# Performance work log

Measured on AMD Instinct MI355X. Metric: run time of the kernel, lower is better.

Reference implementation:

```python
import jax, jax.numpy as jnp
import numpy as np

D_MODEL = 1024
N_HEADS = 16
D_K = D_MODEL // N_HEADS


def setup_inputs() -> dict:
    key = jax.random.key(0)
    ks = jax.random.split(key, 11)
    B, S = 2, 2048
    scale = 1.0 / np.sqrt(D_MODEL)
    inp = {
        "Q_in": jax.random.normal(ks[0], (B, S, D_MODEL), jnp.float32),
        "K_in": jax.random.normal(ks[1], (B, S, D_MODEL), jnp.float32),
        "V_in": jax.random.normal(ks[2], (B, S, D_MODEL), jnp.float32),
        # torch nn.Linear convention: y = x @ W.T + b, W shape [out, in]
        "W_q": jax.random.normal(ks[3], (D_MODEL, D_MODEL), jnp.float32) * scale,
        "b_q": jax.random.normal(ks[4], (D_MODEL,), jnp.float32) * scale,
        "W_k": jax.random.normal(ks[5], (D_MODEL, D_MODEL), jnp.float32) * scale,
        "b_k": jax.random.normal(ks[6], (D_MODEL,), jnp.float32) * scale,
        "W_v": jax.random.normal(ks[7], (D_MODEL, D_MODEL), jnp.float32) * scale,
        "b_v": jax.random.normal(ks[8], (D_MODEL,), jnp.float32) * scale,
        "W_o": jax.random.normal(ks[9], (D_MODEL, D_MODEL), jnp.float32) * scale,
        "b_o": jax.random.normal(ks[10], (D_MODEL,), jnp.float32) * scale,
    }
    return inp


def reference(Q_in, K_in, V_in, W_q, b_q, W_k, b_k, W_v, b_v, W_o, b_o):
    B, S, _ = Q_in.shape

    def proj(x, W, b):
        # [B,S,D] -> [B,H,S,dk]
        y = x @ W.T + b
        return y.reshape(B, S, N_HEADS, D_K).transpose(0, 2, 1, 3)

    Q = proj(Q_in, W_q, b_q)
    K = proj(K_in, W_k, b_k)
    V = proj(V_in, W_v, b_v)

    scores = jnp.einsum("bhqd,bhkd->bhqk", Q, K) / jnp.sqrt(jnp.float32(D_K))
    attn_weights = jax.nn.softmax(scores, axis=-1)
    ctx = jnp.einsum("bhqk,bhkd->bhqd", attn_weights, V)
    ctx = ctx.transpose(0, 2, 1, 3).reshape(B, S, D_MODEL)
    output = ctx @ W_o.T + b_o
    return output, attn_weights
```

## Files before the change

kernel.cpp:

```cpp
#include <hip/hip_runtime.h>
#include <hip/hip_bf16.h>
#include <stdint.h>

typedef __attribute__((ext_vector_type(8))) short short8;
typedef __attribute__((ext_vector_type(4))) short short4v;
typedef __attribute__((ext_vector_type(4))) float f32x4;
typedef __attribute__((ext_vector_type(2))) float f32x2;

#define MFMA16x16x32(A, B, C) __builtin_amdgcn_mfma_f32_16x16x32_bf16((A), (B), (C), 0, 0, 0)

static constexpr int kS  = 2048;
static constexpr int kD  = 1024;
static constexpr int kDK = 64;

static constexpr size_t OFF_XQ  = 0;
static constexpr size_t OFF_XK  = 4194304;
static constexpr size_t OFF_XV  = 8388608;
static constexpr size_t OFF_W   = 12582912;
static constexpr size_t OFF_QP  = 16777216;
static constexpr size_t OFF_KP  = 20971520;
static constexpr size_t OFF_VT  = 25165824;
static constexpr size_t OFF_CTX = 29360128;

__device__ __forceinline__ short f2bf(float f) {
  __hip_bfloat16 h = __float2bfloat16(f);
  return *reinterpret_cast<short*>(&h);
}

__global__ __launch_bounds__(256) void cvt_kernel(
    const float* __restrict__ xq, const float* __restrict__ xk, const float* __restrict__ xv,
    const float* __restrict__ wq, const float* __restrict__ wk, const float* __restrict__ wv,
    const float* __restrict__ wo, __hip_bfloat16* __restrict__ dst)
{
  int g = blockIdx.x * 256 + threadIdx.x;
  const float* src;
  __hip_bfloat16* d;
  int rel;
  if (g < 3145728) {
    int seg = g >> 20; rel = g & 1048575;
    src = seg == 0 ? xq : (seg == 1 ? xk : xv);
    d = dst + (size_t)seg * 4194304;
  } else {
    int g2 = g - 3145728; int seg = g2 >> 18; rel = g2 & 262143;
    src = seg == 0 ? wq : (seg == 1 ? wk : (seg == 2 ? wv : wo));
    d = dst + OFF_W + (size_t)seg * 1048576;
  }
  float4 v = ((const float4*)src)[rel];
  short4v o;
  o.x = f2bf(v.x); o.y = f2bf(v.y); o.z = f2bf(v.z); o.w = f2bf(v.w);
  ((short4v*)d)[rel] = o;
}

__device__ __forceinline__ void stage_tile(short* lds, const __hip_bfloat16* g0, int t) {
  #pragma unroll
  for (int c = 0; c < 2; ++c) {
    const int e = t * 8 + c * 2048;
    const int row = e >> 5;
    const int kk = e & 31;
    __builtin_amdgcn_global_load_lds(
        (const __attribute__((address_space(1))) void*)(g0 + (size_t)row * kD + kk),
        (__attribute__((address_space(3))) void*)(lds + e), 16, 0, 0);
  }
}

__device__ __forceinline__ void gemm_main(const __hip_bfloat16* X, const __hip_bfloat16* W,
                                          short* As, short* Bs, f32x4 acc[4][4])
{
  const int t = threadIdx.x;
  const int lane = t & 63;
  const int wv = t >> 6;
  const int wr = wv >> 1, wc = wv & 1;
  const int fr = lane & 15;
  const int fc = (lane >> 4) * 8;
  for (int k0 = 0; k0 < kD; k0 += 32) {
    stage_tile(As, X + k0, t);
    stage_tile(Bs, W + k0, t);
    __syncthreads();
    short8 af[4], bfv[4];
    #pragma unroll
    for (int i = 0; i < 4; ++i) af[i]  = *(const short8*)&As[(wr * 64 + i * 16 + fr) * 32 + fc];
    #pragma unroll
    for (int i = 0; i < 4; ++i) bfv[i] = *(const short8*)&Bs[(wc * 64 + i * 16 + fr) * 32 + fc];
    #pragma unroll
    for (int i = 0; i < 4; ++i)
      #pragma unroll
      for (int j = 0; j < 4; ++j)
        acc[i][j] = MFMA16x16x32(af[i], bfv[j], acc[i][j]);
    __syncthreads();
  }
}

__global__ __launch_bounds__(256) void qkv_gemm(
    const __hip_bfloat16* __restrict__ Xq, const __hip_bfloat16* __restrict__ Xk,
    const __hip_bfloat16* __restrict__ Xv, const __hip_bfloat16* __restrict__ Wbase,
    const float* __restrict__ bq, const float* __restrict__ bk, const float* __restrict__ bv,
    __hip_bfloat16* __restrict__ Qp, __hip_bfloat16* __restrict__ Kp,
    __hip_bfloat16* __restrict__ Vt)
{
  __shared__ __align__(16) short As[128 * 32];
  __shared__ __align__(16) short Bs[128 * 32];
  const int z  = blockIdx.z;
  const int m0 = blockIdx.y * 128, n0 = blockIdx.x * 128;
  const __hip_bfloat16* X = (z == 0 ? Xq : (z == 1 ? Xk : Xv)) + (size_t)m0 * kD;
  const __hip_bfloat16* W = Wbase + (size_t)z * (kD * kD) + (size_t)n0 * kD;
  const float* bias = (z == 0 ? bq : (z == 1 ? bk : bv));
  f32x4 acc[4][4] = {};
  gemm_main(X, W, As, Bs, acc);

  const int lane = threadIdx.x & 63;
  const int wv = threadIdx.x >> 6;
  const int wr = wv >> 1, wc = wv & 1;
  short* dstQK = (short*)(z == 0 ? Qp : Kp);
  short* dstV  = (short*)Vt;
  #pragma unroll
  for (int i = 0; i < 4; ++i) {
    #pragma unroll
    for (int j = 0; j < 4; ++j) {
      #pragma unroll
      for (int r = 0; r < 4; ++r) {
        int m = m0 + wr * 64 + i * 16 + (lane >> 4) * 4 + r;
        int n = n0 + wc * 64 + j * 16 + (lane & 15);
        float y = acc[i][j][r] + bias[n];
        if (z == 0) y *= 0.125f;
        int b = m >> 11, sq = m & 2047, h = n >> 6, d = n & 63;
        if (z < 2)
          dstQK[((size_t)(b * 16 + h) * kS + sq) * kDK + d] = f2bf(y);
        else
          dstV[((size_t)(b * 16 + h) * kDK + d) * kS + sq] = f2bf(y);
      }
    }
  }
}

__global__ __launch_bounds__(256) void o_gemm(
    const __hip_bfloat16* __restrict__ Ctx, const __hip_bfloat16* __restrict__ Wo,
    const float* __restrict__ bo, float* __restrict__ out)
{
  __shared__ __align__(16) short As[128 * 32];
  __shared__ __align__(16) short Bs[128 * 32];
  const int m0 = blockIdx.y * 128, n0 = blockIdx.x * 128;
  f32x4 acc[4][4] = {};
  gemm_main(Ctx + (size_t)m0 * kD, Wo + (size_t)n0 * kD, As, Bs, acc);

  const int lane = threadIdx.x & 63;
  const int wv = threadIdx.x >> 6;
  const int wr = wv >> 1, wc = wv & 1;
  #pragma unroll
  for (int i = 0; i < 4; ++i) {
    #pragma unroll
    for (int j = 0; j < 4; ++j) {
      #pragma unroll
      for (int r = 0; r < 4; ++r) {
        int m = m0 + wr * 64 + i * 16 + (lane >> 4) * 4 + r;
        int n = n0 + wc * 64 + j * 16 + (lane & 15);
        __builtin_nontemporal_store(acc[i][j][r] + bo[n], &out[(size_t)m * kD + n]);
      }
    }
  }
}

__global__ __launch_bounds__(256) void attn_pass1(
    const __hip_bfloat16* __restrict__ Qp, const __hip_bfloat16* __restrict__ Kp,
    const __hip_bfloat16* __restrict__ Vt, __hip_bfloat16* __restrict__ Ctx,
    float* __restrict__ rinvp)
{
  __shared__ __align__(16) short Ks[2][32][68];
  __shared__ __align__(16) short Vs[2][64][36];
  __shared__ __align__(16) short Ps[4][16][36];
  const int t = threadIdx.x;
  const int lane = t & 63;
  const int w = t >> 6;
  const int fr = lane & 15;
  const int g4 = lane >> 4;
  const int fc = g4 * 8;

  const int id  = blockIdx.x;
  const int swz = (id & 7) * 128 + (id >> 3);
  const int bh  = swz >> 5;
  const int q0  = (swz & 31) * 64 + w * 16;

  const __hip_bfloat16* Qh = Qp + (size_t)bh * kS * kDK;
  const __hip_bfloat16* Kh = Kp + (size_t)bh * kS * kDK;
  const __hip_bfloat16* Vh = Vt + (size_t)bh * kDK * kS;

  const short8 qf0 = *(const short8*)(Qh + (size_t)(q0 + fr) * kDK + fc);
  const short8 qf1 = *(const short8*)(Qh + (size_t)(q0 + fr) * kDK + 32 + fc);

  const int kr = t >> 3, kc = (t & 7) * 8;
  const int vr = t >> 2, vc = (t & 3) * 8;

  f32x4 ctxacc[4] = {};
  float ssumq = 0.f;

  short8 kA, vA, kB, vB;

#define LOAD_T(KREG, VREG, TI)                                                   \
  KREG = *(const short8*)(Kh + (size_t)((TI) * 32 + kr) * kDK + kc);             \
  VREG = *(const short8*)(Vh + (size_t)vr * kS + (TI) * 32 + vc);

#define STORE_T(KREG, VREG, BUF)                                                 \
  *(short8*)&Ks[BUF][kr][kc] = KREG;                                             \
  *(short8*)&Vs[BUF][vr][vc] = VREG;

#define COMPUTE_T(BUF)                                                           \
  {                                                                              \
    short8 k0a = *(const short8*)&Ks[BUF][fr][fc];                               \
    short8 k0b = *(const short8*)&Ks[BUF][fr][32 + fc];                          \
    short8 k1a = *(const short8*)&Ks[BUF][16 + fr][fc];                          \
    short8 k1b = *(const short8*)&Ks[BUF][16 + fr][32 + fc];                     \
    f32x4 s0 = {}; s0 = MFMA16x16x32(k0a, qf0, s0); s0 = MFMA16x16x32(k0b, qf1, s0); \
    f32x4 s1 = {}; s1 = MFMA16x16x32(k1a, qf0, s1); s1 = MFMA16x16x32(k1b, qf1, s1); \
    float e00 = __expf(s0[0]), e01 = __expf(s0[1]);                              \
    float e02 = __expf(s0[2]), e03 = __expf(s0[3]);                              \
    float e10 = __expf(s1[0]), e11 = __expf(s1[1]);                              \
    float e12 = __expf(s1[2]), e13 = __expf(s1[3]);                              \
    ssumq += (e00 + e01) + (e02 + e03) + (e10 + e11) + (e12 + e13);              \
    short4v p0, p1;                                                              \
    p0.x = f2bf(e00); p0.y = f2bf(e01); p0.z = f2bf(e02); p0.w = f2bf(e03);      \
    p1.x = f2bf(e10); p1.y = f2bf(e11); p1.z = f2bf(e12); p1.w = f2bf(e13);      \
    *(short4v*)&Ps[w][fr][g4 * 4]      = p0;                                     \
    *(short4v*)&Ps[w][fr][16 + g4 * 4] = p1;                                     \
    short8 pf = *(const short8*)&Ps[w][fr][fc];                                  \
    _Pragma("unroll")                                                            \
    for (int dc = 0; dc < 4; ++dc) {                                             \
      short8 vf = *(const short8*)&Vs[BUF][dc * 16 + fr][fc];                    \
      ctxacc[dc] = MFMA16x16x32(pf, vf, ctxacc[dc]);                             \
    }                                                                            \
  }

  LOAD_T(kA, vA, 0);
  STORE_T(kA, vA, 0);
  LOAD_T(kB, vB, 1);
  __syncthreads();

  for (int i = 0; i < 64; i += 2) {
    COMPUTE_T(0);
    STORE_T(kB, vB, 1);
    if (i + 2 < 64) { LOAD_T(kA, vA, i + 2); }
    __syncthreads();
    COMPUTE_T(1);
    if (i + 2 < 64) { STORE_T(kA, vA, 0); }
    if (i + 3 < 64) { LOAD_T(kB, vB, i + 3); }
    __syncthreads();
  }

  float s = ssumq;
  s += __shfl_xor(s, 16);
  s += __shfl_xor(s, 32);
  const float rvq = 1.0f / s;
  if (g4 == 0) rinvp[(size_t)bh * kS + q0 + fr] = rvq;

  float rinv4[4];
  #pragma unroll
  for (int j = 0; j < 4; ++j) rinv4[j] = __shfl(rvq, g4 * 4 + j, 16);

  const int b = bh >> 4, h = bh & 15;
  #pragma unroll
  for (int dc = 0; dc < 4; ++dc) {
    #pragma unroll
    for (int j = 0; j < 4; ++j) {
      int r = g4 * 4 + j;
      float v = ctxacc[dc][j] * rinv4[j];
      ((short*)Ctx)[((size_t)(b * kS + q0 + r)) * kD + h * kDK + dc * 16 + fr] = f2bf(v);
    }
  }
#undef LOAD_T
#undef STORE_T
#undef COMPUTE_T
}

__global__ __launch_bounds__(256) void attn_pass2(
    const __hip_bfloat16* __restrict__ Qp, const __hip_bfloat16* __restrict__ Kp,
    const float* __restrict__ rinvp, float* __restrict__ Aw)
{
  const int t = threadIdx.x;
  const int lane = t & 63;
  const int w = t >> 6;
  const int fr = lane & 15;
  const int g4 = lane >> 4;
  const int fc = g4 * 8;

  const int id  = blockIdx.x;
  const int swz = (id & 7) * 512 + (id >> 3);
  const int bh  = swz >> 7;
  const int ksg = (swz >> 5) & 3;
  const int q0  = (swz & 31) * 64 + w * 16;
  const int k0  = ksg * 512;

  const __hip_bfloat16* Qh = Qp + (size_t)bh * kS * kDK;
  const __hip_bfloat16* Kh = Kp + (size_t)bh * kS * kDK;

  const short8 qf0 = *(const short8*)(Qh + (size_t)(q0 + fr) * kDK + fc);
  const short8 qf1 = *(const short8*)(Qh + (size_t)(q0 + fr) * kDK + 32 + fc);

  const float rvq = rinvp[(size_t)bh * kS + q0 + fr];
  float* aw = Aw + ((size_t)bh * kS + q0 + fr) * kS;

  short8 ka[8], kb[8];

#define LOADK(ARR, KT_)                                                          \
  _Pragma("unroll")                                                              \
  for (int c = 0; c < 4; ++c) {                                                  \
    ARR[2 * c]     = *(const short8*)(Kh + (size_t)((KT_) + c * 16 + fr) * kDK + fc);      \
    ARR[2 * c + 1] = *(const short8*)(Kh + (size_t)((KT_) + c * 16 + fr) * kDK + 32 + fc); \
  }

#define CSTORE(ARR, KT_)                                                         \
  _Pragma("unroll")                                                              \
  for (int c = 0; c < 4; ++c) {                                                  \
    f32x4 st = {};                                                               \
    st = MFMA16x16x32(ARR[2 * c], qf0, st);                                      \
    st = MFMA16x16x32(ARR[2 * c + 1], qf1, st);                                  \
    f32x4 v;                                                                     \
    _Pragma("unroll")                                                            \
    for (int j = 0; j < 4; ++j) v[j] = __expf(st[j]) * rvq;                      \
    __builtin_nontemporal_store(v, (f32x4*)(aw + (KT_) + c * 16 + g4 * 4));      \
  }

  LOADK(ka, k0);
  for (int kt = k0; kt < k0 + 512; kt += 128) {
    LOADK(kb, kt + 64);
    CSTORE(ka, kt);
    if (kt + 128 < k0 + 512) { LOADK(ka, kt + 128); }
    CSTORE(kb, kt + 64);
  }
#undef LOADK
#undef CSTORE
}

extern "C" void kernel_launch(void* const* d_in, const int* in_sizes, int n_in,
                              void* d_out, int out_size, void* d_ws, size_t ws_size,
                              hipStream_t stream) {
  (void)in_sizes; (void)n_in; (void)out_size; (void)ws_size;
  const float* Qin = (const float*)d_in[0];
  const float* Kin = (const float*)d_in[1];
  const float* Vin = (const float*)d_in[2];
  const float* Wq  = (const float*)d_in[3];
  const float* bq  = (const float*)d_in[4];
  const float* Wk  = (const float*)d_in[5];
  const float* bk  = (const float*)d_in[6];
  const float* Wv  = (const float*)d_in[7];
  const float* bv  = (const float*)d_in[8];
  const float* Wo  = (const float*)d_in[9];
  const float* bo  = (const float*)d_in[10];
  __hip_bfloat16* ws = (__hip_bfloat16*)d_ws;
  float* out = (float*)d_out;
  float* rinvp = (float*)(ws + OFF_XQ);

  cvt_kernel<<<16384, 256, 0, stream>>>(Qin, Kin, Vin, Wq, Wk, Wv, Wo, ws);
  qkv_gemm<<<dim3(8, 32, 3), 256, 0, stream>>>(
      ws + OFF_XQ, ws + OFF_XK, ws + OFF_XV, ws + OFF_W, bq, bk, bv,
      ws + OFF_QP, ws + OFF_KP, ws + OFF_VT);
  attn_pass1<<<1024, 256, 0, stream>>>(
      ws + OFF_QP, ws + OFF_KP, ws + OFF_VT, ws + OFF_CTX, rinvp);
  attn_pass2<<<4096, 256, 0, stream>>>(
      ws + OFF_QP, ws + OFF_KP, rinvp, out + 4194304);
  o_gemm<<<dim3(8, 32), 256, 0, stream>>>(
      ws + OFF_CTX, ws + OFF_W + 3 * 1048576, bo, out);
}
```

Measured before the change: 298.8 us.

## Load K/V directly into registers in attention pass and fuse O-GEMM with pass2

```diff
diff --git a/kernel.cpp b/kernel.cpp
--- a/kernel.cpp
+++ b/kernel.cpp
@@ -132,40 +132,11 @@
   }
 }
 
-__global__ __launch_bounds__(256) void o_gemm(
-    const __hip_bfloat16* __restrict__ Ctx, const __hip_bfloat16* __restrict__ Wo,
-    const float* __restrict__ bo, float* __restrict__ out)
-{
-  __shared__ __align__(16) short As[128 * 32];
-  __shared__ __align__(16) short Bs[128 * 32];
-  const int m0 = blockIdx.y * 128, n0 = blockIdx.x * 128;
-  f32x4 acc[4][4] = {};
-  gemm_main(Ctx + (size_t)m0 * kD, Wo + (size_t)n0 * kD, As, Bs, acc);
-
-  const int lane = threadIdx.x & 63;
-  const int wv = threadIdx.x >> 6;
-  const int wr = wv >> 1, wc = wv & 1;
-  #pragma unroll
-  for (int i = 0; i < 4; ++i) {
-    #pragma unroll
-    for (int j = 0; j < 4; ++j) {
-      #pragma unroll
-      for (int r = 0; r < 4; ++r) {
-        int m = m0 + wr * 64 + i * 16 + (lane >> 4) * 4 + r;
-        int n = n0 + wc * 64 + j * 16 + (lane & 15);
-        __builtin_nontemporal_store(acc[i][j][r] + bo[n], &out[(size_t)m * kD + n]);
-      }
-    }
-  }
-}
-
 __global__ __launch_bounds__(256) void attn_pass1(
     const __hip_bfloat16* __restrict__ Qp, const __hip_bfloat16* __restrict__ Kp,
     const __hip_bfloat16* __restrict__ Vt, __hip_bfloat16* __restrict__ Ctx,
     float* __restrict__ rinvp)
 {
-  __shared__ __align__(16) short Ks[2][32][68];
-  __shared__ __align__(16) short Vs[2][64][36];
   __shared__ __align__(16) short Ps[4][16][36];
   const int t = threadIdx.x;
   const int lane = t & 63;
@@ -186,30 +157,24 @@
   const short8 qf0 = *(const short8*)(Qh + (size_t)(q0 + fr) * kDK + fc);
   const short8 qf1 = *(const short8*)(Qh + (size_t)(q0 + fr) * kDK + 32 + fc);
 
-  const int kr = t >> 3, kc = (t & 7) * 8;
-  const int vr = t >> 2, vc = (t & 3) * 8;
-
   f32x4 ctxacc[4] = {};
   float ssumq = 0.f;
 
-  short8 kA, vA, kB, vB;
-
-#define LOAD_T(KREG, VREG, TI)                                                   \
-  KREG = *(const short8*)(Kh + (size_t)((TI) * 32 + kr) * kDK + kc);             \
-  VREG = *(const short8*)(Vh + (size_t)vr * kS + (TI) * 32 + vc);
-
-#define STORE_T(KREG, VREG, BUF)                                                 \
-  *(short8*)&Ks[BUF][kr][kc] = KREG;                                             \
-  *(short8*)&Vs[BUF][vr][vc] = VREG;
-
-#define COMPUTE_T(BUF)                                                           \
+  short8 kA[4], vA[4], kB[4], vB[4];
+
+#define LOAD32(KR, VR, KT_)                                                      \
+  KR[0] = *(const short8*)(Kh + (size_t)((KT_) + fr) * kDK + fc);                \
+  KR[1] = *(const short8*)(Kh + (size_t)((KT_) + fr) * kDK + 32 + fc);           \
+  KR[2] = *(const short8*)(Kh + (size_t)((KT_) + 16 + fr) * kDK + fc);           \
+  KR[3] = *(const short8*)(Kh + (size_t)((KT_) + 16 + fr) * kDK + 32 + fc);      \
+  _Pragma("unroll")                                                              \
+  for (int dc = 0; dc < 4; ++dc)                                                 \
+    VR[dc] = *(const short8*)(Vh + (size_t)(dc * 16 + fr) * kS + (KT_) + fc);
+
+#define COMPUTE32(KR, VR)                                                        \
   {                                                                              \
-    short8 k0a = *(const short8*)&Ks[BUF][fr][fc];                               \
-    short8 k0b = *(const short8*)&Ks[BUF][fr][32 + fc];                          \
-    short8 k1a = *(const short8*)&Ks[BUF][16 + fr][fc];                          \
-    short8 k1b = *(const short8*)&Ks[BUF][16 + fr][32 + fc];                     \
-    f32x4 s0 = {}; s0 = MFMA16x16x32(k0a, qf0, s0); s0 = MFMA16x16x32(k0b, qf1, s0); \
-    f32x4 s1 = {}; s1 = MFMA16x16x32(k1a, qf0, s1); s1 = MFMA16x16x32(k1b, qf1, s1); \
+    f32x4 s0 = {}; s0 = MFMA16x16x32(KR[0], qf0, s0); s0 = MFMA16x16x32(KR[1], qf1, s0); \
+    f32x4 s1 = {}; s1 = MFMA16x16x32(KR[2], qf0, s1); s1 = MFMA16x16x32(KR[3], qf1, s1); \
     float e00 = __expf(s0[0]), e01 = __expf(s0[1]);                              \
     float e02 = __expf(s0[2]), e03 = __expf(s0[3]);                              \
     float e10 = __expf(s1[0]), e11 = __expf(s1[1]);                              \
@@ -222,27 +187,19 @@
     *(short4v*)&Ps[w][fr][16 + g4 * 4] = p1;                                     \
     short8 pf = *(const short8*)&Ps[w][fr][fc];                                  \
     _Pragma("unroll")                                                            \
-    for (int dc = 0; dc < 4; ++dc) {                                             \
-      short8 vf = *(const short8*)&Vs[BUF][dc * 16 + fr][fc];                    \
-      ctxacc[dc] = MFMA16x16x32(pf, vf, ctxacc[dc]);                             \
-    }                                                                            \
-  }
-
-  LOAD_T(kA, vA, 0);
-  STORE_T(kA, vA, 0);
-  LOAD_T(kB, vB, 1);
-  __syncthreads();
-
-  for (int i = 0; i < 64; i += 2) {
-    COMPUTE_T(0);
-    STORE_T(kB, vB, 1);
-    if (i + 2 < 64) { LOAD_T(kA, vA, i + 2); }
-    __syncthreads();
-    COMPUTE_T(1);
-    if (i + 2 < 64) { STORE_T(kA, vA, 0); }
-    if (i + 3 < 64) { LOAD_T(kB, vB, i + 3); }
-    __syncthreads();
-  }
+    for (int dc = 0; dc < 4; ++dc)                                               \
+      ctxacc[dc] = MFMA16x16x32(pf, VR[dc], ctxacc[dc]);                         \
+  }
+
+  LOAD32(kA, vA, 0);
+  for (int kt = 0; kt < kS; kt += 64) {
+    LOAD32(kB, vB, kt + 32);
+    COMPUTE32(kA, vA);
+    if (kt + 64 < kS) { LOAD32(kA, vA, kt + 64); }
+    COMPUTE32(kB, vB);
+  }
+#undef LOAD32
+#undef COMPUTE32
 
   float s = ssumq;
   s += __shfl_xor(s, 16);
@@ -264,15 +221,16 @@
       ((short*)Ctx)[((size_t)(b * kS + q0 + r)) * kD + h * kDK + dc * 16 + fr] = f2bf(v);
     }
   }
-#undef LOAD_T
-#undef STORE_T
-#undef COMPUTE_T
-}
-
-__global__ __launch_bounds__(256) void attn_pass2(
+}
+
+__global__ __launch_bounds__(256) void fused_tail(
+    const __hip_bfloat16* __restrict__ Ctx, const __hip_bfloat16* __restrict__ Wo,
+    const float* __restrict__ bo, float* __restrict__ out,
     const __hip_bfloat16* __restrict__ Qp, const __hip_bfloat16* __restrict__ Kp,
     const float* __restrict__ rinvp, float* __restrict__ Aw)
 {
+  __shared__ __align__(16) short As[128 * 32];
+  __shared__ __align__(16) short Bs[128 * 32];
   const int t = threadIdx.x;
   const int lane = t & 63;
   const int w = t >> 6;
@@ -280,7 +238,27 @@
   const int g4 = lane >> 4;
   const int fc = g4 * 8;
 
-  const int id  = blockIdx.x;
+  if (blockIdx.x < 256) {
+    const int m0 = (blockIdx.x >> 3) * 128, n0 = (blockIdx.x & 7) * 128;
+    f32x4 acc[4][4] = {};
+    gemm_main(Ctx + (size_t)m0 * kD, Wo + (size_t)n0 * kD, As, Bs, acc);
+    const int wr = w >> 1, wc = w & 1;
+    #pragma unroll
+    for (int i = 0; i < 4; ++i) {
+      #pragma unroll
+      for (int j = 0; j < 4; ++j) {
+        #pragma unroll
+        for (int r = 0; r < 4; ++r) {
+          int m = m0 + wr * 64 + i * 16 + g4 * 4 + r;
+          int n = n0 + wc * 64 + j * 16 + fr;
+          __builtin_nontemporal_store(acc[i][j][r] + bo[n], &out[(size_t)m * kD + n]);
+        }
+      }
+    }
+    return;
+  }
+
+  const int id  = blockIdx.x - 256;
   const int swz = (id & 7) * 512 + (id >> 3);
   const int bh  = swz >> 7;
   const int ksg = (swz >> 5) & 3;
@@ -353,8 +331,7 @@
       ws + OFF_QP, ws + OFF_KP, ws + OFF_VT);
   attn_pass1<<<1024, 256, 0, stream>>>(
       ws + OFF_QP, ws + OFF_KP, ws + OFF_VT, ws + OFF_CTX, rinvp);
-  attn_pass2<<<4096, 256, 0, stream>>>(
+  fused_tail<<<4352, 256, 0, stream>>>(
+      ws + OFF_CTX, ws + OFF_W + 3 * 1048576, bo, out,
       ws + OFF_QP, ws + OFF_KP, rinvp, out + 4194304);
-  o_gemm<<<dim3(8, 32), 256, 0, stream>>>(
-      ws + OFF_CTX, ws + OFF_W + 3 * 1048576, bo, out);
-}
+}
```

Result: slower. 450.6 us (+50.8%).

## Compute softmax row sums first, then fuse attention-weight writes into PV pass

Applied to the files above, without the earlier changes.

```diff
diff --git a/kernel.cpp b/kernel.cpp
--- a/kernel.cpp
+++ b/kernel.cpp
@@ -159,10 +159,69 @@
   }
 }
 
-__global__ __launch_bounds__(256) void attn_pass1(
+__global__ __launch_bounds__(256) void attn_pass0(
+    const __hip_bfloat16* __restrict__ Qp, const __hip_bfloat16* __restrict__ Kp,
+    float* __restrict__ partp)
+{
+  const int t = threadIdx.x;
+  const int lane = t & 63;
+  const int w = t >> 6;
+  const int fr = lane & 15;
+  const int g4 = lane >> 4;
+  const int fc = g4 * 8;
+
+  const int id  = blockIdx.x;
+  const int swz = (id & 7) * 256 + (id >> 3);
+  const int bh  = swz >> 6;
+  const int ksg = (swz >> 5) & 1;
+  const int q0  = (swz & 31) * 64 + w * 16;
+  const int k0  = ksg * 1024;
+
+  const __hip_bfloat16* Qh = Qp + (size_t)bh * kS * kDK;
+  const __hip_bfloat16* Kh = Kp + (size_t)bh * kS * kDK;
+
+  const short8 qf0 = *(const short8*)(Qh + (size_t)(q0 + fr) * kDK + fc);
+  const short8 qf1 = *(const short8*)(Qh + (size_t)(q0 + fr) * kDK + 32 + fc);
+
+  float ssumq = 0.f;
+  short8 ka[8], kb[8];
+
+#define LOADK(ARR, KT_)                                                          \
+  _Pragma("unroll")                                                              \
+  for (int c = 0; c < 4; ++c) {                                                  \
+    ARR[2 * c]     = *(const short8*)(Kh + (size_t)((KT_) + c * 16 + fr) * kDK + fc);      \
+    ARR[2 * c + 1] = *(const short8*)(Kh + (size_t)((KT_) + c * 16 + fr) * kDK + 32 + fc); \
+  }
+
+#define CACC(ARR)                                                                \
+  _Pragma("unroll")                                                              \
+  for (int c = 0; c < 4; ++c) {                                                  \
+    f32x4 st = {};                                                               \
+    st = MFMA16x16x32(ARR[2 * c], qf0, st);                                      \
+    st = MFMA16x16x32(ARR[2 * c + 1], qf1, st);                                  \
+    ssumq += (__expf(st[0]) + __expf(st[1])) + (__expf(st[2]) + __expf(st[3]));  \
+  }
+
+  LOADK(ka, k0);
+  for (int kt = k0; kt < k0 + 1024; kt += 128) {
+    LOADK(kb, kt + 64);
+    CACC(ka);
+    if (kt + 128 < k0 + 1024) { LOADK(ka, kt + 128); }
+    CACC(kb);
+  }
+#undef LOADK
+#undef CACC
+
+  float s = ssumq;
+  s += __shfl_xor(s, 16);
+  s += __shfl_xor(s, 32);
+  if (g4 == 0) partp[((size_t)bh * 2 + ksg) * kS + q0 + fr] = s;
+}
+
+__global__ __launch_bounds__(256) void attn_main(
     const __hip_bfloat16* __restrict__ Qp, const __hip_bfloat16* __restrict__ Kp,
     const __hip_bfloat16* __restrict__ Vt, __hip_bfloat16* __restrict__ Ctx,
-    float* __restrict__ rinvp)
+    const float* __restrict__ partp, float* __restrict__ Aw)
 {
   __shared__ __align__(16) short Ks[2][32][68];
   __shared__ __align__(16) short Vs[2][64][36];
@@ -186,11 +245,18 @@
   const short8 qf0 = *(const short8*)(Qh + (size_t)(q0 + fr) * kDK + fc);
   const short8 qf1 = *(const short8*)(Qh + (size_t)(q0 + fr) * kDK + 32 + fc);
 
+  const float rvq = 1.0f / (partp[(size_t)bh * 2 * kS + q0 + fr] +
+                            partp[((size_t)bh * 2 + 1) * kS + q0 + fr]);
+  float rinv4[4];
+  #pragma unroll
+  for (int j = 0; j < 4; ++j) rinv4[j] = __shfl(rvq, g4 * 4 + j, 16);
+
+  float* aw = Aw + ((size_t)bh * kS + q0 + fr) * kS;
+
   const int kr = t >> 3, kc = (t & 7) * 8;
   const int vr = t >> 2, vc = (t & 3) * 8;
 
   f32x4 ctxacc[4] = {};
-  float ssumq = 0.f;
 
   short8 kA, vA, kB, vB;
 
@@ -202,7 +268,7 @@
   *(short8*)&Ks[BUF][kr][kc] = KREG;                                             \
   *(short8*)&Vs[BUF][vr][vc] = VREG;
 
-#define COMPUTE_T(BUF)                                                           \
+#define COMPUTE_T(BUF, KT_)                                                      \
   {                                                                              \
     short8 k0a = *(const short8*)&Ks[BUF][fr][fc];                               \
     short8 k0b = *(const short8*)&Ks[BUF][fr][32 + fc];                          \
@@ -214,7 +280,11 @@
     float e02 = __expf(s0[2]), e03 = __expf(s0[3]);                              \
     float e10 = __expf(s1[0]), e11 = __expf(s1[1]);                              \
     float e12 = __expf(s1[2]), e13 = __expf(s1[3]);                              \
-    ssumq += (e00 + e01) + (e02 + e03) + (e10 + e11) + (e12 + e13);              \
+    f32x4 w0, w1;                                                                \
+    w0[0] = e00 * rvq; w0[1] = e01 * rvq; w0[2] = e02 * rvq; w0[3] = e03 * rvq;  \
+    w1[0] = e10 * rvq; w1[1] = e11 * rvq; w1[2] = e12 * rvq; w1[3] = e13 * rvq;  \
+    __builtin_nontemporal_store(w0, (f32x4*)(aw + (KT_) + g4 * 4));              \
+    __builtin_nontemporal_store(w1, (f32x4*)(aw + (KT_) + 16 + g4 * 4));         \
     short4v p0, p1;                                                              \
     p0.x = f2bf(e00); p0.y = f2bf(e01); p0.z = f2bf(e02); p0.w = f2bf(e03);      \
     p1.x = f2bf(e10); p1.y = f2bf(e11); p1.z = f2bf(e12); p1.w = f2bf(e13);      \
@@ -234,25 +304,15 @@
   __syncthreads();
 
   for (int i = 0; i < 64; i += 2) {
-    COMPUTE_T(0);
+    COMPUTE_T(0, i * 32);
     STORE_T(kB, vB, 1);
     if (i + 2 < 64) { LOAD_T(kA, vA, i + 2); }
     __syncthreads();
-    COMPUTE_T(1);
+    COMPUTE_T(1, (i + 1) * 32);
     if (i + 2 < 64) { STORE_T(kA, vA, 0); }
     if (i + 3 < 64) { LOAD_T(kB, vB, i + 3); }
     __syncthreads();
   }
-
-  float s = ssumq;
-  s += __shfl_xor(s, 16);
-  s += __shfl_xor(s, 32);
-  const float rvq = 1.0f / s;
-  if (g4 == 0) rinvp[(size_t)bh * kS + q0 + fr] = rvq;
-
-  float rinv4[4];
-  #pragma unroll
-  for (int j = 0; j < 4; ++j) rinv4[j] = __shfl(rvq, g4 * 4 + j, 16);
 
   const int b = bh >> 4, h = bh & 15;
   #pragma unroll
@@ -267,65 +327,6 @@
 #undef LOAD_T
 #undef STORE_T
 #undef COMPUTE_T
-}
-
-__global__ __launch_bounds__(256) void attn_pass2(
-    const __hip_bfloat16* __restrict__ Qp, const __hip_bfloat16* __restrict__ Kp,
-    const float* __restrict__ rinvp, float* __restrict__ Aw)
-{
-  const int t = threadIdx.x;
-  const int lane = t & 63;
-  const int w = t >> 6;
-  const int fr = lane & 15;
-  const int g4 = lane >> 4;
-  const int fc = g4 * 8;
-
-  const int id  = blockIdx.x;
-  const int swz = (id & 7) * 512 + (id >> 3);
-  const int bh  = swz >> 7;
-  const int ksg = (swz >> 5) & 3;
-  const int q0  = (swz & 31) * 64 + w * 16;
-  const int k0  = ksg * 512;
-
-  const __hip_bfloat16* Qh = Qp + (size_t)bh * kS * kDK;
-  const __hip_bfloat16* Kh = Kp + (size_t)bh * kS * kDK;
-
-  const short8 qf0 = *(const short8*)(Qh + (size_t)(q0 + fr) * kDK + fc);
-  const short8 qf1 = *(const short8*)(Qh + (size_t)(q0 + fr) * kDK + 32 + fc);
-
-  const float rvq = rinvp[(size_t)bh * kS + q0 + fr];
-  float* aw = Aw + ((size_t)bh * kS + q0 + fr) * kS;
-
-  short8 ka[8], kb[8];
-
-#define LOADK(ARR, KT_)                                                          \
-  _Pragma("unroll")                                                              \
-  for (int c = 0; c < 4; ++c) {                                                  \
-    ARR[2 * c]     = *(const short8*)(Kh + (size_t)((KT_) + c * 16 + fr) * kDK + fc);      \
-    ARR[2 * c + 1] = *(const short8*)(Kh + (size_t)((KT_) + c * 16 + fr) * kDK + 32 + fc); \
-  }
-
-#define CSTORE(ARR, KT_)                                                         \
-  _Pragma("unroll")                                                              \
-  for (int c = 0; c < 4; ++c) {                                                  \
-    f32x4 st = {};                                                               \
-    st = MFMA16x16x32(ARR[2 * c], qf0, st);                                      \
-    st = MFMA16x16x32(ARR[2 * c + 1], qf1, st);                                  \
-    f32x4 v;                                                                     \
-    _Pragma("unroll")                                                            \
-    for (int j = 0; j < 4; ++j) v[j] = __expf(st[j]) * rvq;                      \
-    __builtin_nontemporal_store(v, (f32x4*)(aw + (KT_) + c * 16 + g4 * 4));      \
-  }
-
-  LOADK(ka, k0);
-  for (int kt = k0; kt < k0 + 512; kt += 128) {
-    LOADK(kb, kt + 64);
-    CSTORE(ka, kt);
-    if (kt + 128 < k0 + 512) { LOADK(ka, kt + 128); }
-    CSTORE(kb, kt + 64);
-  }
-#undef LOADK
-#undef CSTORE
 }
 
 extern "C" void kernel_launch(void* const* d_in, const int* in_sizes, int n_in,
@@ -345,16 +346,15 @@
   const float* bo  = (const float*)d_in[10];
   __hip_bfloat16* ws = (__hip_bfloat16*)d_ws;
   float* out = (float*)d_out;
-  float* rinvp = (float*)(ws + OFF_XQ);
+  float* partp = (float*)(ws + OFF_XQ);
 
   cvt_kernel<<<16384, 256, 0, stream>>>(Qin, Kin, Vin, Wq, Wk, Wv, Wo, ws);
   qkv_gemm<<<dim3(8, 32, 3), 256, 0, stream>>>(
       ws + OFF_XQ, ws + OFF_XK, ws + OFF_XV, ws + OFF_W, bq, bk, bv,
       ws + OFF_QP, ws + OFF_KP, ws + OFF_VT);
-  attn_pass1<<<1024, 256, 0, stream>>>(
-      ws + OFF_QP, ws + OFF_KP, ws + OFF_VT, ws + OFF_CTX, rinvp);
-  attn_pass2<<<4096, 256, 0, stream>>>(
-      ws + OFF_QP, ws + OFF_KP, rinvp, out + 4194304);
+  attn_pass0<<<2048, 256, 0, stream>>>(ws + OFF_QP, ws + OFF_KP, partp);
+  attn_main<<<1024, 256, 0, stream>>>(
+      ws + OFF_QP, ws + OFF_KP, ws + OFF_VT, ws + OFF_CTX, partp, out + 4194304);
   o_gemm<<<dim3(8, 32), 256, 0, stream>>>(
       ws + OFF_CTX, ws + OFF_W + 3 * 1048576, bo, out);
 }
```

New measurement: 371.1 us. 24.2% more time.
